# Kernel optimization log

Hardware: AMD Instinct MI355X
Metric: run time of the kernel (lower is better)

## Reference

```python
import jax, jax.numpy as jnp
import numpy as np

N, IN, OUT = 8192, 4096, 4096
GROUP = 4
ACT_BITS = 8


def setup_inputs() -> dict:
    key = jax.random.key(0)
    k_x, k_w, k_b = jax.random.split(key, 3)
    input = jax.random.normal(k_x, (N, IN), dtype=jnp.float32)
    # ternary weights in {-1, 0, +1}, stored as float for compute
    weight = jax.random.randint(k_w, (OUT, IN), -1, 2).astype(jnp.float32)
    weight_scale = jnp.ones((1,), dtype=jnp.float32) * 0.02
    bias = jax.random.normal(k_b, (OUT,), dtype=jnp.float32) * 0.01
    return {"input": input, "weight": weight, "weight_scale": weight_scale, "bias": bias}


def reference(input, weight, weight_scale, bias):
    n, in_f = input.shape
    out_f = weight.shape[0]
    qmax = 2 ** (ACT_BITS - 1) - 1  # 127
    # absmax activation quantization (inference path)
    act_scale = jnp.abs(input).max() / qmax
    x_q = jnp.clip(jnp.round(input / act_scale), -(qmax + 1), qmax)
    # LUT path math: per 4-wide group, contribution = sum(w_group) * mean(x_group)
    g = in_f // GROUP
    x_mean = x_q.reshape(n, g, GROUP).mean(axis=-1)          # [N, G]
    w_sum = weight.reshape(out_f, g, GROUP).sum(axis=-1)     # [OUT, G]
    out = jnp.einsum('ng,og->no', x_mean, w_sum)
    out = out * weight_scale * act_scale + bias
    return out
```

## Files before the change

### kernel.cpp

```cpp
#include <hip/hip_runtime.h>
#include <hip/hip_bf16.h>

#define NROWS 8192
#define INF   4096
#define OUTF  4096
#define G     1024

typedef _Float16 f16x8 __attribute__((ext_vector_type(8)));
typedef float    f32x4 __attribute__((ext_vector_type(4)));


__global__ void absmax_part(const float4* __restrict__ x,
                            float* __restrict__ partial) {
    const int stride = 1024 * 256;
    int i = blockIdx.x * 256 + threadIdx.x;
    float m = 0.f;
    #pragma unroll 4
    for (int it = 0; it < 32; ++it, i += stride) {
        float4 v = x[i];
        m = fmaxf(m, fmaxf(fmaxf(fabsf(v.x), fabsf(v.y)),
                           fmaxf(fabsf(v.z), fabsf(v.w))));
    }
    for (int off = 32; off; off >>= 1)
        m = fmaxf(m, __shfl_down(m, off));
    __shared__ float wm[4];
    int lane = threadIdx.x & 63, wave = threadIdx.x >> 6;
    if (lane == 0) wm[wave] = m;
    __syncthreads();
    if (threadIdx.x == 0)
        partial[blockIdx.x] = fmaxf(fmaxf(wm[0], wm[1]), fmaxf(wm[2], wm[3]));
}

__global__ void absmax_final(const float* __restrict__ partial,
                             float* __restrict__ scale_out) {
    int t = threadIdx.x;
    float m = fmaxf(fmaxf(partial[t], partial[t + 256]),
                    fmaxf(partial[t + 512], partial[t + 768]));
    for (int off = 32; off; off >>= 1)
        m = fmaxf(m, __shfl_down(m, off));
    __shared__ float wm[4];
    int lane = t & 63, wave = t >> 6;
    if (lane == 0) wm[wave] = m;
    __syncthreads();
    if (t == 0) {
        float bm = fmaxf(fmaxf(wm[0], wm[1]), fmaxf(wm[2], wm[3]));
        scale_out[0] = bm * (1.0f / 127.0f);
    }
}

__global__ void prep_fused(const float4* __restrict__ x,
                           const float4* __restrict__ w,
                           const float* __restrict__ scale_p,
                           _Float16* __restrict__ xs,
                           _Float16* __restrict__ ws) {
    const int b = blockIdx.x;
    const int t = threadIdx.x;
    if (b < 16384) {
        const float s = scale_p[0];
        int i0 = b * 512 + t;
        #pragma unroll
        for (int u = 0; u < 2; ++u) {
            int i = i0 + u * 256;
            float4 v = x[i];
            float q0 = fminf(fmaxf(rintf(v.x / s), -128.f), 127.f);
            float q1 = fminf(fmaxf(rintf(v.y / s), -128.f), 127.f);
            float q2 = fminf(fmaxf(rintf(v.z / s), -128.f), 127.f);
            float q3 = fminf(fmaxf(rintf(v.w / s), -128.f), 127.f);
            xs[i] = (_Float16)(q0 + q1 + q2 + q3);
        }
    } else {
        int i0 = (b - 16384) * 512 + t;
        #pragma unroll
        for (int u = 0; u < 2; ++u) {
            int i = i0 + u * 256;
            float4 v = w[i];
            ws[i] = (_Float16)(v.x + v.y + v.z + v.w);
        }
    }
}

#define BM 256
#define BN 128
#define BK 32

__device__ __forceinline__ void async_copy16(const void* g, void* l) {
    __builtin_amdgcn_global_load_lds(
        (const __attribute__((address_space(1))) unsigned int*)g,
        (__attribute__((address_space(3))) unsigned int*)l,
        16, 0, 0);
}

__global__ __launch_bounds__(256, 2) void gemm_kernel(
    const _Float16* __restrict__ A,
    const _Float16* __restrict__ B,
    const float* __restrict__ bias,
    const float* __restrict__ scale_p,
    const float* __restrict__ wscale,
    float* __restrict__ out) {

    __shared__ alignas(16) _Float16 As[BM * BK];
    __shared__ alignas(16) _Float16 Bs[BN * BK];

    const int t = threadIdx.x;
    const int lane = t & 63;
    const int wave = t >> 6;
    const int wm = (wave >> 1) * 128;
    const int wn = (wave & 1) * 64;

    const long rowA0 = (long)blockIdx.y * BM;
    const long rowB0 = (long)blockIdx.x * BN;

    f32x4 acc[8][4] = {};

    const int srow = lane >> 2;
    const int scol = (lane & 3) * 8;

    for (int k0 = 0; k0 < G; k0 += BK) {
        __syncthreads();
        #pragma unroll
        for (int i = 0; i < 6; ++i) {
            const int c = wave * 6 + i;
            if (c < 16) {
                const int row = c * 16 + srow;
                async_copy16(A + (rowA0 + row) * (long)G + k0 + scol, As + c * 512);
            } else {
                const int row = (c - 16) * 16 + srow;
                async_copy16(B + (rowB0 + row) * (long)G + k0 + scol, Bs + (c - 16) * 512);
            }
        }
        __syncthreads();

        f16x8 af[8], bf[4];
        #pragma unroll
        for (int mi = 0; mi < 8; ++mi)
            af[mi] = *(const f16x8*)&As[(wm + mi * 16 + (lane & 15)) * BK + (lane >> 4) * 8];
        #pragma unroll
        for (int nj = 0; nj < 4; ++nj)
            bf[nj] = *(const f16x8*)&Bs[(wn + nj * 16 + (lane & 15)) * BK + (lane >> 4) * 8];

        #pragma unroll
        for (int mi = 0; mi < 8; ++mi)
            #pragma unroll
            for (int nj = 0; nj < 4; ++nj)
                acc[mi][nj] = __builtin_amdgcn_mfma_f32_16x16x32_f16(
                    af[mi], bf[nj], acc[mi][nj], 0, 0, 0);
    }

    const float scale = scale_p[0] * 0.25f * wscale[0];
    const int r0 = (int)rowA0 + wm + (lane >> 4) * 4;
    const int c0 = (int)rowB0 + wn + (lane & 15);
    #pragma unroll
    for (int nj = 0; nj < 4; ++nj) {
        const int col = c0 + nj * 16;
        const float b = bias[col];
        #pragma unroll
        for (int mi = 0; mi < 8; ++mi) {
            const int row = r0 + mi * 16;
            #pragma unroll
            for (int r = 0; r < 4; ++r)
                out[(long)(row + r) * OUTF + col] = acc[mi][nj][r] * scale + b;
        }
    }
}

extern "C" void kernel_launch(void* const* d_in, const int* in_sizes, int n_in,
                              void* d_out, int out_size, void* d_ws, size_t ws_size,
                              hipStream_t stream) {
    const float* input  = (const float*)d_in[0];
    const float* weight = (const float*)d_in[1];
    const float* wscale = (const float*)d_in[2];
    const float* bias   = (const float*)d_in[3];
    float* out = (float*)d_out;

    float* act_scale = (float*)d_ws;
    float* partials  = (float*)((char*)d_ws + 16);
    _Float16* x_sum  = (_Float16*)((char*)d_ws + 8192);
    _Float16* w_sum  = (_Float16*)((char*)d_ws + 8192 + (size_t)NROWS * G * 2);

    absmax_part<<<1024, 256, 0, stream>>>((const float4*)input, partials);
    absmax_final<<<1, 256, 0, stream>>>(partials, act_scale);
    prep_fused<<<24576, 256, 0, stream>>>((const float4*)input, (const float4*)weight,
                                          act_scale, x_sum, w_sum);
    gemm_kernel<<<dim3(OUTF / BN, NROWS / BM), 256, 0, stream>>>(
        x_sum, w_sum, bias, act_scale, wscale, out);
}
```

Baseline: 375.9 us.

## Double-buffer GEMM LDS tiles with swizzle and fold weight sums into absmax pass

```diff
diff --git a/kernel.cpp b/kernel.cpp
--- a/kernel.cpp
+++ b/kernel.cpp
@@ -1,5 +1,4 @@
 #include <hip/hip_runtime.h>
-#include <hip/hip_bf16.h>
 
 #define NROWS 8192
 #define INF   4096
@@ -10,32 +9,48 @@
 typedef float    f32x4 __attribute__((ext_vector_type(4)));
 
 
-__global__ void absmax_part(const float4* __restrict__ x,
-                            float* __restrict__ partial) {
-    const int stride = 1024 * 256;
-    int i = blockIdx.x * 256 + threadIdx.x;
-    float m = 0.f;
-    #pragma unroll 4
-    for (int it = 0; it < 32; ++it, i += stride) {
-        float4 v = x[i];
-        m = fmaxf(m, fmaxf(fmaxf(fabsf(v.x), fabsf(v.y)),
-                           fmaxf(fabsf(v.z), fabsf(v.w))));
+__global__ void pass1(const float4* __restrict__ x,
+                      const float4* __restrict__ w,
+                      float* __restrict__ partial,
+                      _Float16* __restrict__ ws) {
+    const int t = threadIdx.x;
+    const int b = blockIdx.x;
+    if (b < 2048) {
+        const int stride = 2048 * 256;
+        int i = b * 256 + t;
+        float m = 0.f;
+        #pragma unroll 4
+        for (int it = 0; it < 16; ++it, i += stride) {
+            float4 v = x[i];
+            m = fmaxf(m, fmaxf(fmaxf(fabsf(v.x), fabsf(v.y)),
+                               fmaxf(fabsf(v.z), fabsf(v.w))));
+        }
+        for (int off = 32; off; off >>= 1)
+            m = fmaxf(m, __shfl_down(m, off));
+        __shared__ float wm[4];
+        int lane = t & 63, wave = t >> 6;
+        if (lane == 0) wm[wave] = m;
+        __syncthreads();
+        if (t == 0)
+            partial[b] = fmaxf(fmaxf(wm[0], wm[1]), fmaxf(wm[2], wm[3]));
+    } else {
+        int i = (b - 2048) * 4096 + t;
+        #pragma unroll 4
+        for (int it = 0; it < 16; ++it, i += 256) {
+            float4 v = w[i];
+            ws[i] = (_Float16)(v.x + v.y + v.z + v.w);
+        }
     }
-    for (int off = 32; off; off >>= 1)
-        m = fmaxf(m, __shfl_down(m, off));
-    __shared__ float wm[4];
-    int lane = threadIdx.x & 63, wave = threadIdx.x >> 6;
-    if (lane == 0) wm[wave] = m;
-    __syncthreads();
-    if (threadIdx.x == 0)
-        partial[blockIdx.x] = fmaxf(fmaxf(wm[0], wm[1]), fmaxf(wm[2], wm[3]));
 }
 
 __global__ void absmax_final(const float* __restrict__ partial,
-                             float* __restrict__ scale_out) {
+                             const float* __restrict__ wscale,
+                             float* __restrict__ sc) {
     int t = threadIdx.x;
-    float m = fmaxf(fmaxf(partial[t], partial[t + 256]),
-                    fmaxf(partial[t + 512], partial[t + 768]));
+    float m = 0.f;
+    #pragma unroll
+    for (int u = 0; u < 8; ++u)
+        m = fmaxf(m, partial[t + u * 256]);
     for (int off = 32; off; off >>= 1)
         m = fmaxf(m, __shfl_down(m, off));
     __shared__ float wm[4];
@@ -44,38 +59,24 @@
     __syncthreads();
     if (t == 0) {
         float bm = fmaxf(fmaxf(wm[0], wm[1]), fmaxf(wm[2], wm[3]));
-        scale_out[0] = bm * (1.0f / 127.0f);
+        float s = bm * (1.0f / 127.0f);
+        sc[0] = s;
+        sc[1] = 127.0f / bm;
+        sc[2] = s * 0.25f * wscale[0];
     }
 }
 
-__global__ void prep_fused(const float4* __restrict__ x,
-                           const float4* __restrict__ w,
-                           const float* __restrict__ scale_p,
-                           _Float16* __restrict__ xs,
-                           _Float16* __restrict__ ws) {
-    const int b = blockIdx.x;
-    const int t = threadIdx.x;
-    if (b < 16384) {
-        const float s = scale_p[0];
-        int i0 = b * 512 + t;
-        #pragma unroll
-        for (int u = 0; u < 2; ++u) {
-            int i = i0 + u * 256;
-            float4 v = x[i];
-            float q0 = fminf(fmaxf(rintf(v.x / s), -128.f), 127.f);
-            float q1 = fminf(fmaxf(rintf(v.y / s), -128.f), 127.f);
-            float q2 = fminf(fmaxf(rintf(v.z / s), -128.f), 127.f);
-            float q3 = fminf(fmaxf(rintf(v.w / s), -128.f), 127.f);
-            xs[i] = (_Float16)(q0 + q1 + q2 + q3);
-        }
-    } else {
-        int i0 = (b - 16384) * 512 + t;
-        #pragma unroll
-        for (int u = 0; u < 2; ++u) {
-            int i = i0 + u * 256;
-            float4 v = w[i];
-            ws[i] = (_Float16)(v.x + v.y + v.z + v.w);
-        }
+__global__ void xquant(const float4* __restrict__ x,
+                       const float* __restrict__ sc,
+                       _Float16* __restrict__ xs) {
+    const float inv = sc[1];
+    int i0 = blockIdx.x * 512 + threadIdx.x;
+    #pragma unroll
+    for (int u = 0; u < 2; ++u) {
+        int i = i0 + u * 256;
+        float4 v = x[i];
+        xs[i] = (_Float16)(rintf(v.x * inv) + rintf(v.y * inv) +
+                           rintf(v.z * inv) + rintf(v.w * inv));
     }
 }
 
@@ -94,12 +95,11 @@
     const _Float16* __restrict__ A,
     const _Float16* __restrict__ B,
     const float* __restrict__ bias,
-    const float* __restrict__ scale_p,
-    const float* __restrict__ wscale,
+    const float* __restrict__ sc,
     float* __restrict__ out) {
 
-    __shared__ alignas(16) _Float16 As[BM * BK];
-    __shared__ alignas(16) _Float16 Bs[BN * BK];
+    __shared__ alignas(16) _Float16 As[2][BM * BK];
+    __shared__ alignas(16) _Float16 Bs[2][BN * BK];
 
     const int t = threadIdx.x;
     const int lane = t & 63;
@@ -113,30 +113,39 @@
     f32x4 acc[8][4] = {};
 
     const int srow = lane >> 2;
-    const int scol = (lane & 3) * 8;
+    const int scol = ((lane & 3) << 3) ^ (((lane >> 3) & 3) << 3);
+    const int swzR = ((lane >> 1) & 3) << 3;
 
-    for (int k0 = 0; k0 < G; k0 += BK) {
-        __syncthreads();
+    auto stage = [&](int buf, int k0) {
         #pragma unroll
         for (int i = 0; i < 6; ++i) {
             const int c = wave * 6 + i;
             if (c < 16) {
                 const int row = c * 16 + srow;
-                async_copy16(A + (rowA0 + row) * (long)G + k0 + scol, As + c * 512);
+                async_copy16(A + (rowA0 + row) * (long)G + k0 + scol, &As[buf][c * 512]);
             } else {
                 const int row = (c - 16) * 16 + srow;
-                async_copy16(B + (rowB0 + row) * (long)G + k0 + scol, Bs + (c - 16) * 512);
+                async_copy16(B + (rowB0 + row) * (long)G + k0 + scol, &Bs[buf][(c - 16) * 512]);
             }
         }
-        __syncthreads();
+    };
+
+    stage(0, 0);
+    __syncthreads();
+
+    int cur = 0;
+    for (int ks = 0; ks < G / BK; ++ks) {
+        if (ks + 1 < G / BK) stage(cur ^ 1, (ks + 1) * BK);
 
         f16x8 af[8], bf[4];
         #pragma unroll
         for (int mi = 0; mi < 8; ++mi)
-            af[mi] = *(const f16x8*)&As[(wm + mi * 16 + (lane & 15)) * BK + (lane >> 4) * 8];
+            af[mi] = *(const f16x8*)&As[cur][(wm + mi * 16 + (lane & 15)) * BK
+                                            + (((lane >> 4) * 8) ^ swzR)];
         #pragma unroll
         for (int nj = 0; nj < 4; ++nj)
-            bf[nj] = *(const f16x8*)&Bs[(wn + nj * 16 + (lane & 15)) * BK + (lane >> 4) * 8];
+            bf[nj] = *(const f16x8*)&Bs[cur][(wn + nj * 16 + (lane & 15)) * BK
+                                            + (((lane >> 4) * 8) ^ swzR)];
 
         #pragma unroll
         for (int mi = 0; mi < 8; ++mi)
@@ -144,9 +153,12 @@
             for (int nj = 0; nj < 4; ++nj)
                 acc[mi][nj] = __builtin_amdgcn_mfma_f32_16x16x32_f16(
                     af[mi], bf[nj], acc[mi][nj], 0, 0, 0);
+
+        __syncthreads();
+        cur ^= 1;
     }
 
-    const float scale = scale_p[0] * 0.25f * wscale[0];
+    const float scale = sc[2];
     const int r0 = (int)rowA0 + wm + (lane >> 4) * 4;
     const int c0 = (int)rowB0 + wn + (lane & 15);
     #pragma unroll
@@ -172,15 +184,15 @@
     const float* bias   = (const float*)d_in[3];
     float* out = (float*)d_out;
 
-    float* act_scale = (float*)d_ws;
-    float* partials  = (float*)((char*)d_ws + 16);
-    _Float16* x_sum  = (_Float16*)((char*)d_ws + 8192);
-    _Float16* w_sum  = (_Float16*)((char*)d_ws + 8192 + (size_t)NROWS * G * 2);
+    float* scales   = (float*)d_ws;
+    float* partials = (float*)((char*)d_ws + 16);
+    _Float16* x_sum = (_Float16*)((char*)d_ws + 8208);
+    _Float16* w_sum = (_Float16*)((char*)d_ws + 8208 + (size_t)NROWS * G * 2);
 
-    absmax_part<<<1024, 256, 0, stream>>>((const float4*)input, partials);
-    absmax_final<<<1, 256, 0, stream>>>(partials, act_scale);
-    prep_fused<<<24576, 256, 0, stream>>>((const float4*)input, (const float4*)weight,
-                                          act_scale, x_sum, w_sum);
+    pass1<<<3072, 256, 0, stream>>>((const float4*)input, (const float4*)weight,
+                                    partials, w_sum);
+    absmax_final<<<1, 256, 0, stream>>>(partials, wscale, scales);
+    xquant<<<16384, 256, 0, stream>>>((const float4*)input, scales, x_sum);
     gemm_kernel<<<dim3(OUTF / BN, NROWS / BM), 256, 0, stream>>>(
-        x_sum, w_sum, bias, act_scale, wscale, out);
+        x_sum, w_sum, bias, scales, out);
 }
```

After: 386.5 us. 2.8% more time.
